# Kernel optimization log

Measured on AMD Instinct MI355X. Metric: run time of the kernel, lower is better.

The kernel has to match this reference:

```python
import jax, jax.numpy as jnp
import numpy as np

B, T, D_MODEL = 2, 2048, 2048
N, H, R = 1024, 16, 512
DH = 128          # mem_head_dim (even, fully rotated: rope_dim == DH)
MLAT = 128        # mem_latent_dim
TOPK = 64
EPS = 1e-6
ROPE_BASE = 10000.0


def _rms_norm(x, w):
    var = jnp.mean(jnp.square(x), axis=-1, keepdims=True)
    return x * jax.lax.rsqrt(var + EPS) * w


def _rotate_half(x):
    x1, x2 = jnp.split(x, 2, axis=-1)
    return jnp.concatenate([-x2, x1], axis=-1)


def _apply_rope(x, positions):
    # x: [B, H, L, DH], positions: [L] -> cos/sin [1, 1, L, DH]
    inv_freq = 1.0 / (ROPE_BASE ** (jnp.arange(0, DH, 2, dtype=jnp.float32) / DH))
    freqs = positions.astype(jnp.float32)[:, None] * inv_freq  # [L, DH/2]
    emb = jnp.concatenate([freqs, freqs], axis=-1)             # [L, DH]
    cos = jnp.cos(emb)[None, None].astype(x.dtype)
    sin = jnp.sin(emb)[None, None].astype(x.dtype)
    return x * cos + _rotate_half(x) * sin


def setup_inputs() -> dict:
    key = jax.random.key(0)
    ks = jax.random.split(key, 16)
    s = 0.02
    return {
        "x": jax.random.normal(ks[0], (B, T, D_MODEL), jnp.float32),
        "snapshots": jax.random.normal(ks[1], (B, N, H, R), jnp.float32),
        "snap_positions": jnp.sort(jax.random.randint(ks[2], (N,), 0, T)),
        "token_offset": 0,
        "Wq_down": jax.random.normal(ks[3], (D_MODEL, MLAT), jnp.float32) * s,
        "Wq_up": jax.random.normal(ks[4], (MLAT, H * DH), jnp.float32) * s,
        "Wg_down": jax.random.normal(ks[5], (D_MODEL, MLAT), jnp.float32) * s,
        "Wg_up": jax.random.normal(ks[6], (MLAT, H * DH), jnp.float32) * s,
        "Wo_down": jax.random.normal(ks[7], (H * DH, MLAT), jnp.float32) * s,
        "Wo_up": jax.random.normal(ks[8], (MLAT, D_MODEL), jnp.float32) * s,
        "Wk_up": jax.random.normal(ks[9], (R, DH), jnp.float32) * s,
        "Wv_up": jax.random.normal(ks[10], (R, DH), jnp.float32) * s,
        "q_norm_w": jnp.ones((DH,), jnp.float32),
        "k_norm_w": jnp.ones((DH,), jnp.float32),
        "sink_logit": jnp.zeros((H,), jnp.float32),
    }


def reference(x, snapshots, snap_positions, token_offset,
              Wq_down, Wq_up, Wg_down, Wg_up, Wo_down, Wo_up,
              Wk_up, Wv_up, q_norm_w, k_norm_w, sink_logit):
    b, t, d = x.shape
    _, n, h, r = snapshots.shape
    dh = DH

    # Q path: down/up projection, per-head RMSNorm -> [B, H, T, DH]
    q = ((x @ Wq_down) @ Wq_up).reshape(b, t, h, dh)
    q = _rms_norm(q, q_norm_w).transpose(0, 2, 1, 3)

    # K/V from snapshot latents: [B, N, H, DH] -> [B, H, N, DH]
    k = _rms_norm(snapshots @ Wk_up, k_norm_w).transpose(0, 2, 1, 3)
    v = (snapshots @ Wv_up).transpose(0, 2, 1, 3)

    # dual RoPE: Q by absolute token position, K by snapshot end position
    t_abs = token_offset + jnp.arange(t)
    q = _apply_rope(q, t_abs)
    k = _apply_rope(k, snap_positions)

    scores = jnp.einsum('bhtd,bhnd->bhtn', q, k) / jnp.sqrt(jnp.asarray(dh, q.dtype))

    # causal mask: snapshot strictly before token
    valid = (snap_positions[None, :] < t_abs[:, None])[None, None]  # [1,1,T,N]
    neg_inf = jnp.asarray(-jnp.inf, scores.dtype)
    scores = jnp.where(valid, scores, neg_inf)

    # causal top-k: keep entries >= k-th largest per (b,h,t)
    k_sel = min(TOPK, n)
    if k_sel < n:
        top_vals, _ = jax.lax.top_k(scores, k_sel)
        kth = top_vals[..., -1:]
        scores = jnp.where(scores >= kth, scores, neg_inf)

    # attention sink: extra learned logit per head
    sink = jnp.broadcast_to(sink_logit.astype(jnp.float32)[None, :, None, None], (b, h, t, 1))
    aug = jnp.concatenate([scores.astype(jnp.float32), sink], axis=-1)
    weights = jax.nn.softmax(aug, axis=-1)[..., :n].astype(v.dtype)

    out = jnp.einsum('bhtn,bhnd->bhtd', weights, v)
    out = out.transpose(0, 2, 1, 3).reshape(b, t, h * dh)

    gate = jax.nn.sigmoid((x @ Wg_down) @ Wg_up)
    out = out * gate
    out = (out @ Wo_down) @ Wo_up
    return out
```

## Files before the change

### kernel.cpp

```cpp
#include <hip/hip_runtime.h>

typedef unsigned short u16;
typedef unsigned int u32;
typedef __attribute__((ext_vector_type(8))) short bf16x8;
typedef __attribute__((ext_vector_type(8))) _Float16 f16x8;
typedef __attribute__((ext_vector_type(4))) float f32x4;

__device__ __forceinline__ float b2f(u16 u) {
  union { u32 i; float f; } v; v.i = ((u32)u) << 16; return v.f;
}
__device__ __forceinline__ u16 f2b(float f) {
  u32 u = __builtin_bit_cast(u32, f);
  u32 r = u + 0x7FFFu + ((u >> 16) & 1u);
  return (u16)(r >> 16);
}
__device__ __forceinline__ u16 f2h(float f) {
  return __builtin_bit_cast(u16, (_Float16)f);
}
__device__ __forceinline__ float h2f(u16 u) {
  return (float)__builtin_bit_cast(_Float16, u);
}
__device__ __forceinline__ float wsum(float v) {
  #pragma unroll
  for (int o = 32; o; o >>= 1) v += __shfl_xor(v, o);
  return v;
}
__device__ __forceinline__ float wmax(float v) {
  #pragma unroll
  for (int o = 32; o; o >>= 1) v = fmaxf(v, __shfl_xor(v, o));
  return v;
}

__global__ void k_detect(const u32* x, int* flag) {
  int lane = threadIdx.x;
  u32 w = x[lane * 131 + 7];
  float v = b2f((u16)(w & 0xFFFF));
  float a = fabsf(v);
  bool sane = (a > 1e-3f) && (a < 100.0f);
  unsigned long long m = __ballot(sane);
  if (lane == 0) flag[0] = (__popcll(m) >= 32) ? 0 : 1;
}

struct WtArgs {
  const void* s[8];
  const void* vq; const void* vk; const void* vs;
};
__global__ __launch_bounds__(256)
void k_wtrans_all(WtArgs a, u16* wb, const int* flag) {
  __shared__ u16 Ts[64][66];
  int id = blockIdx.x, t = threadIdx.x, dt = flag[0];
  if (id == 416) {
    u16* dq = wb + 1703936; u16* dk = wb + 1704064; u16* ds = wb + 1704192;
    if (t < 128) dq[t] = dt ? f2b(((const float*)a.vq)[t]) : ((const u16*)a.vq)[t];
    else if (t < 256) dk[t-128] = dt ? f2b(((const float*)a.vk)[t-128]) : ((const u16*)a.vk)[t-128];
    if (t < 16) ds[t] = dt ? f2b(((const float*)a.vs)[t]) : ((const u16*)a.vs)[t];
    return;
  }
  const int cum[9] = {0,64,128,144,160,224,288,352,416};
  const int gsh[8] = {1,1,1,1,5,5,1,5};
  const int Ks[8]  = {2048,2048,512,512,128,128,2048,128};
  const int Ns[8]  = {128,128,128,128,2048,2048,128,2048};
  const unsigned dsts[8] = {0,262144,524288,589824,655360,917504,1179648,1441792};
  int seg = 0;
  #pragma unroll
  for (int i = 0; i < 7; ++i) seg += (id >= cum[i+1]);
  int rel = id - cum[seg];
  int bx = rel & ((1 << gsh[seg]) - 1), by = rel >> gsh[seg];
  int K = Ks[seg], N = Ns[seg];
  const void* src = a.s[seg];
  u16* dst = wb + dsts[seg];
  int col0 = bx * 64, k0 = by * 64;
  int lr = t >> 4, lc = (t & 15) * 4;
  if (dt) {
    #pragma unroll
    for (int p = 0; p < 4; ++p) {
      int kr = lr + p * 16;
      float4 v = *(const float4*)((const float*)src + (size_t)(k0 + kr) * N + col0 + lc);
      Ts[kr][lc+0] = f2b(v.x); Ts[kr][lc+1] = f2b(v.y);
      Ts[kr][lc+2] = f2b(v.z); Ts[kr][lc+3] = f2b(v.w);
    }
  } else {
    #pragma unroll
    for (int p = 0; p < 4; ++p) {
      int kr = lr + p * 16;
      uint2 v = *(const uint2*)((const u16*)src + (size_t)(k0 + kr) * N + col0 + lc);
      *(uint2*)&Ts[kr][lc] = v;
    }
  }
  __syncthreads();
  int col = t >> 2, ks = (t & 3) * 16;
  u16 tmp[16];
  #pragma unroll
  for (int i = 0; i < 16; ++i) tmp[i] = Ts[ks + i][col];
  u16* dp = dst + (size_t)(col0 + col) * K + k0 + ks;
  *(uint4*)dp = *(uint4*)&tmp[0];
  *(uint4*)(dp + 8) = *(uint4*)&tmp[8];
}

template<int JW>
__device__ __forceinline__ void skinny_body(const void* A, const u16* BT, u16* C0, u16* C1,
    int K, bool a32, int m0, int tid, u16 (*As)[40]) {
  int wave = tid >> 6, lane = tid & 63, quad = lane >> 4, l16 = lane & 15;
  f32x4 acc[JW];
  #pragma unroll
  for (int j = 0; j < JW; ++j) acc[j] = (f32x4){0.f,0.f,0.f,0.f};
  int row32 = tid >> 4, kp32 = (tid & 15) * 2;
  int row16 = tid >> 2, kp16 = (tid & 3) * 8;
  float2 pf32 = {};
  uint4 pf16 = {};
  if (a32) pf32 = *(const float2*)((const float*)A + (size_t)(m0+row32)*K + kp32);
  else if (tid < 64) pf16 = *(const uint4*)((const u16*)A + (size_t)(m0+row16)*K + kp16);
  uint4 bf[JW];
  #pragma unroll
  for (int j = 0; j < JW; ++j) {
    int col = wave*(JW*16) + j*16 + l16;
    bf[j] = *(const uint4*)(BT + (size_t)col*K + quad*8);
  }
  for (int k0 = 0; k0 < K; k0 += 32) {
    if (a32) { As[row32][kp32] = f2b(pf32.x); As[row32][kp32+1] = f2b(pf32.y); }
    else if (tid < 64) *(uint4*)&As[row16][kp16] = pf16;
    __syncthreads();
    int k1 = k0 + 32;
    uint4 bn[JW];
    if (k1 < K) {
      if (a32) pf32 = *(const float2*)((const float*)A + (size_t)(m0+row32)*K + k1 + kp32);
      else if (tid < 64) pf16 = *(const uint4*)((const u16*)A + (size_t)(m0+row16)*K + k1 + kp16);
      #pragma unroll
      for (int j = 0; j < JW; ++j) {
        int col = wave*(JW*16) + j*16 + l16;
        bn[j] = *(const uint4*)(BT + (size_t)col*K + k1 + quad*8);
      }
    }
    bf16x8 af = *(const bf16x8*)&As[l16][quad*8];
    #pragma unroll
    for (int j = 0; j < JW; ++j)
      acc[j] = __builtin_amdgcn_mfma_f32_16x16x32_bf16(af, __builtin_bit_cast(bf16x8, bf[j]), acc[j], 0, 0, 0);
    __syncthreads();
    #pragma unroll
    for (int j = 0; j < JW; ++j) bf[j] = bn[j];
  }
  #pragma unroll
  for (int j = 0; j < JW; ++j) {
    int col = wave*(JW*16) + j*16 + l16;
    u16* Cp = (col < 128) ? C0 : C1;
    int cc = col & 127;
    #pragma unroll
    for (int r = 0; r < 4; ++r)
      Cp[(size_t)(m0 + quad*4 + r)*128 + cc] = f2b(acc[j][r]);
  }
}

__device__ __forceinline__ void gemm_up_body(const u16* A, const u16* BT, void* C, int ldc,
    bool o32, int m0, int n0, int tid, u16 (*As)[40]) {
  int wave = tid >> 6, lane = tid & 63, quad = lane >> 4, l16 = lane & 15;
  f32x4 acc[4] = {};
  int row = tid >> 2, kp = (tid & 3) * 8;
  uint4 pa = *(const uint4*)(A + (size_t)(m0+row)*128 + kp);
  uint4 bf[4];
  #pragma unroll
  for (int j = 0; j < 4; ++j)
    bf[j] = *(const uint4*)(BT + (size_t)(n0 + j*16 + l16)*128 + quad*8);
  #pragma unroll
  for (int k0 = 0; k0 < 128; k0 += 32) {
    *(uint4*)&As[row][kp] = pa;
    __syncthreads();
    uint4 bn[4];
    if (k0 < 96) {
      pa = *(const uint4*)(A + (size_t)(m0+row)*128 + k0 + 32 + kp);
      #pragma unroll
      for (int j = 0; j < 4; ++j)
        bn[j] = *(const uint4*)(BT + (size_t)(n0 + j*16 + l16)*128 + k0 + 32 + quad*8);
    }
    bf16x8 af = *(const bf16x8*)&As[wave*16 + l16][quad*8];
    #pragma unroll
    for (int j = 0; j < 4; ++j)
      acc[j] = __builtin_amdgcn_mfma_f32_16x16x32_bf16(af, __builtin_bit_cast(bf16x8, bf[j]), acc[j], 0, 0, 0);
    __syncthreads();
    #pragma unroll
    for (int j = 0; j < 4; ++j) bf[j] = bn[j];
  }
  #pragma unroll
  for (int j = 0; j < 4; ++j) {
    #pragma unroll
    for (int r = 0; r < 4; ++r) {
      size_t ci = (size_t)(m0 + wave*16 + quad*4 + r)*ldc + n0 + j*16 + l16;
      float v = acc[j][r];
      if (o32) ((float*)C)[ci] = v; else ((u16*)C)[ci] = f2b(v);
    }
  }
}

__device__ __forceinline__ void kpost_body(const u16* kraw, u16* kT, const u16* kw,
                                           const int* spos, int rel, int tid) {
  int wave = tid >> 6, lane = tid & 63;
  int rr = rel * 4 + wave;
  int n = (rr >> 4) & 1023, b = rr >> 14, h = rr & 15;
  size_t base = (size_t)rr * 128;
  float x0 = b2f(kraw[base + lane]);
  float x1 = b2f(kraw[base + lane + 64]);
  float ss = wsum(x0*x0 + x1*x1);
  float inv = rsqrtf(ss * (1.0f/128.0f) + 1e-6f);
  float y0 = x0 * inv * b2f(kw[lane]);
  float y1 = x1 * inv * b2f(kw[lane + 64]);
  float pos = (float)spos[n];
  float invf = __expf(-(float)lane * (9.210340371976184f / 64.0f));
  float sn, cs; sincosf(pos * invf, &sn, &cs);
  size_t ob = ((size_t)(b*16 + h) * 1024 + n) * 128;
  kT[ob + lane]      = f2b(y0*cs - y1*sn);
  kT[ob + lane + 64] = f2b(y1*cs + y0*sn);
}

__device__ __forceinline__ void vtrans_body(const u16* vraw, u16* vtt, int bid, int t,
                                            u16 (*Vs)[136]) {
  int ng = bid & 15, bh = bid >> 4;
  int b = bh >> 4, h = bh & 15;
  int n0 = ng * 64;
  int li = t >> 4, seg = (t & 15) * 8;
  #pragma unroll
  for (int p = 0; p < 4; ++p) {
    int i = li + p * 16;
    size_t row = (size_t)(b*1024 + n0 + i) * 16 + h;
    *(uint4*)&Vs[i][seg] = *(const uint4*)(vraw + row*128 + seg);
  }
  __syncthreads();
  int dh = t >> 1, nh = (t & 1) * 32;
  u16 outv[32];
  #pragma unroll
  for (int i = 0; i < 32; ++i) outv[i] = f2h(b2f(Vs[nh + i][dh]));
  u16* dst = vtt + ((size_t)bh * 128 + dh) * 1024 + n0 + nh;
  *(uint4*)(dst)      = *(uint4*)&outv[0];
  *(uint4*)(dst + 8)  = *(uint4*)&outv[8];
  *(uint4*)(dst + 16) = *(uint4*)&outv[16];
  *(uint4*)(dst + 24) = *(uint4*)&outv[24];
}

__global__ __launch_bounds__(256)
void k_down_all(const void* x, const void* snap, const u16* BdT, const u16* BkvT,
                u16* qlat, u16* glat, u16* kraw, u16* vraw, const int* flag) {
  __shared__ u16 As[16][40];
  int id = blockIdx.x;
  bool a32 = flag[0] != 0;
  if (id < 256) skinny_body<4>(x, BdT, qlat, glat, 2048, a32, id*16, threadIdx.x, As);
  else          skinny_body<4>(snap, BkvT, kraw, vraw, 512, a32, (id-256)*16, threadIdx.x, As);
}

__global__ __launch_bounds__(256)
void k_mid_all(const u16* qlat, const u16* glat, const u16* WquT, const u16* WguT,
               u16* qraw, u16* graw, const u16* kraw, u16* kT, const u16* vraw, u16* vtt,
               const u16* ckw, const int* spos, const int* flag) {
  __shared__ u16 smem[64*136];
  int id = blockIdx.x, tid = threadIdx.x;
  if (id < 4096) {
    u16 (*As)[40] = (u16 (*)[40])smem;
    int rel = id & 2047;
    const u16* A  = (id < 2048) ? qlat : glat;
    const u16* BT = (id < 2048) ? WquT : WguT;
    u16* C        = (id < 2048) ? qraw : graw;
    gemm_up_body(A, BT, C, 2048, false, (rel >> 5) * 64, (rel & 31) * 64, tid, As);
  } else if (id < 12288) {
    kpost_body(kraw, kT, ckw, spos, id - 4096, tid);
  } else {
    vtrans_body(vraw, vtt, id - 12288, tid, (u16 (*)[136])smem);
  }
}

__global__ __launch_bounds__(256)
void k_olat(const u16* Ao, const u16* WodT, u16* olat, const int* flag) {
  __shared__ u16 As[16][40];
  skinny_body<2>(Ao, WodT, olat, olat, 2048, false, blockIdx.x*16, threadIdx.x, As);
}

__global__ __launch_bounds__(256)
void k_gemm_up(const u16* A, const u16* BT, void* C, int ldc, const int* flag, int out_dyn) {
  __shared__ u16 As[64][40];
  gemm_up_body(A, BT, C, ldc, out_dyn && flag[0], blockIdx.y*64, blockIdx.x*64, threadIdx.x, As);
}

__global__ __launch_bounds__(256, 4)
void k_attn(const u16* qraw, const u16* kT, const u16* vtt, const u16* graw,
            const int* spos, const int* tok, const u16* sink, const u16* qw, u16* o) {
  __shared__ u16 sc[16][1032];
  __shared__ int pos_s[1024];
  __shared__ float rz_s[16];
  u16 (*Qs)[136] = (u16 (*)[136])&sc[0][0];

  int tid = threadIdx.x;
  int wave = tid >> 6, lane = tid & 63, quad = lane >> 4, l16 = lane & 15;
  int bid = blockIdx.x;
  int tile = bid & 127, bh = bid >> 7;
  int h = bh & 15, b = bh >> 4;
  int t0 = tile * 16;
  int tok0 = tok[0];

  ((int4*)pos_s)[tid] = ((const int4*)spos)[tid];

  {
    float qw0 = b2f(qw[lane]), qw1 = b2f(qw[lane + 64]);
    float invf = __expf(-(float)lane * (9.210340371976184f / 64.0f));
    #pragma unroll 1
    for (int s = 0; s < 4; ++s) {
      int i = wave*4 + s;
      size_t base = ((size_t)(b*2048 + t0 + i))*2048 + h*128;
      float x0 = b2f(qraw[base + lane]);
      float x1 = b2f(qraw[base + lane + 64]);
      float ss = wsum(x0*x0 + x1*x1);
      float inv = rsqrtf(ss * (1.0f/128.0f) + 1e-6f);
      float y0 = x0 * inv * qw0;
      float y1 = x1 * inv * qw1;
      float pos = (float)(tok0 + t0 + i);
      float sn, cs; sincosf(pos * invf, &sn, &cs);
      Qs[i][lane]      = f2b(y0*cs - y1*sn);
      Qs[i][lane + 64] = f2b(y1*cs + y0*sn);
    }
  }
  __syncthreads();

  int nmax;
  {
    int lim = tok0 + t0 + 15;
    int lo = 0, hi = 1024;
    #pragma unroll 1
    while (lo < hi) { int mid = (lo + hi) >> 1; if (pos_s[mid] < lim) lo = mid + 1; else hi = mid; }
    nmax = lo;
  }
  int pmax = (nmax + 63) >> 6;
  int kkmax = (nmax + 31) >> 5;

  bf16x8 af[4];
  #pragma unroll
  for (int ks = 0; ks < 4; ++ks) af[ks] = *(const bf16x8*)&Qs[l16][ks*32 + quad*8];
  __syncthreads();

  const u16* kTb = kT + (size_t)bh * 131072;
  int nrow = wave*16 + l16;
  uint4 kf[4];
  if (pmax > 0) {
    const u16* kr = kTb + (size_t)nrow * 128 + quad*8;
    #pragma unroll
    for (int ks = 0; ks < 4; ++ks) kf[ks] = *(const uint4*)(kr + ks*32);
  }
  #pragma unroll 1
  for (int p = 0; p < pmax; ++p) {
    uint4 kn[4];
    if (p + 1 < pmax) {
      const u16* kr = kTb + (size_t)((p+1)*64 + nrow) * 128 + quad*8;
      #pragma unroll
      for (int ks = 0; ks < 4; ++ks) kn[ks] = *(const uint4*)(kr + ks*32);
    }
    f32x4 c = {};
    #pragma unroll
    for (int ks = 0; ks < 4; ++ks)
      c = __builtin_amdgcn_mfma_f32_16x16x32_bf16(af[ks], __builtin_bit_cast(bf16x8, kf[ks]), c, 0, 0, 0);
    int n = p*64 + nrow;
    int pn = pos_s[n];
    #pragma unroll
    for (int r = 0; r < 4; ++r) {
      int t = quad*4 + r;
      float s = c[r] * 0.08838834764831845f;
      if (pn >= tok0 + t0 + t) s = -INFINITY;
      sc[t][n] = f2h(s);
    }
    #pragma unroll
    for (int ks = 0; ks < 4; ++ks) kf[ks] = kn[ks];
  }
  #pragma unroll 1
  for (int p = pmax; p < 16; ++p) {
    int n = p*64 + nrow;
    #pragma unroll
    for (int r = 0; r < 4; ++r) sc[quad*4 + r][n] = 0xFC00u;
  }
  __syncthreads();

  float sinkv = b2f(sink[h]);

  #pragma unroll 1
  for (int s5 = 0; s5 < 4; ++s5) {
    int tl = wave*4 + s5;
    uint4 r0 = *(const uint4*)&sc[tl][lane*16];
    uint4 r1 = *(const uint4*)&sc[tl][lane*16 + 8];
    float sv[16]; int key[16];
    float mx = -INFINITY;
    #pragma unroll
    for (int j = 0; j < 16; ++j) {
      u16 hb = (j < 8) ? ((const u16*)&r0)[j] : ((const u16*)&r1)[j-8];
      float f = h2f(hb);
      sv[j] = f; mx = fmaxf(mx, f);
      float fs = fminf(fmaxf(f * 256.0f + 2048.0f, 0.0f), 4095.0f);
      key[j] = (int)fs;
    }
    mx = wmax(mx);
    int lo = 0, hi = 4096;
    #pragma unroll 1
    for (int it = 0; it < 12; ++it) {
      int mid = (lo + hi) >> 1;
      int c = 0;
      #pragma unroll
      for (int j = 0; j < 16; ++j) c += (int)__popcll(__ballot(key[j] >= mid));
      if (c >= 64) lo = mid; else hi = mid;
    }
    float m = fmaxf(mx, sinkv);
    float zp = 0.f;
    u16 wq[16];
    #pragma unroll
    for (int j = 0; j < 16; ++j) {
      float e = (key[j] >= lo && sv[j] > -1e37f) ? __expf(sv[j] - m) : 0.f;
      zp += e;
      wq[j] = f2h(e);
    }
    float Z = wsum(zp) + __expf(sinkv - m);
    if (lane == 0) rz_s[tl] = 1.0f / Z;
    *(uint4*)&sc[tl][lane*16]     = *(uint4*)&wq[0];
    *(uint4*)&sc[tl][lane*16 + 8] = *(uint4*)&wq[8];
  }
  __syncthreads();

  const u16* vbase = vtt + (size_t)bh * 131072;
  int dh0 = wave * 32;
  const u16* vr0 = vbase + (size_t)(dh0 + l16)*1024 + quad*8;
  const u16* vr1 = vbase + (size_t)(dh0 + 16 + l16)*1024 + quad*8;
  f32x4 acc0 = {}, acc1 = {};
  uint4 vf0 = *(const uint4*)vr0;
  uint4 vf1 = *(const uint4*)vr1;
  #pragma unroll 1
  for (int kk = 0; kk < kkmax; ++kk) {
    uint4 vn0, vn1;
    if (kk + 1 < kkmax) {
      vn0 = *(const uint4*)(vr0 + (kk+1)*32);
      vn1 = *(const uint4*)(vr1 + (kk+1)*32);
    }
    f16x8 a = *(const f16x8*)&sc[l16][kk*32 + quad*8];
    acc0 = __builtin_amdgcn_mfma_f32_16x16x32_f16(a, __builtin_bit_cast(f16x8, vf0), acc0, 0, 0, 0);
    acc1 = __builtin_amdgcn_mfma_f32_16x16x32_f16(a, __builtin_bit_cast(f16x8, vf1), acc1, 0, 0, 0);
    vf0 = vn0; vf1 = vn1;
  }

  #pragma unroll
  for (int r = 0; r < 4; ++r) {
    int t = quad*4 + r;
    float rz = rz_s[t];
    size_t oi = ((size_t)(b*2048 + t0 + t))*2048 + h*128 + dh0 + l16;
    float g0 = 1.0f / (1.0f + __expf(-b2f(graw[oi])));
    float g1 = 1.0f / (1.0f + __expf(-b2f(graw[oi + 16])));
    o[oi] = f2b(acc0[r] * rz * g0);
    o[oi + 16] = f2b(acc1[r] * rz * g1);
  }
}

extern "C" void kernel_launch(void* const* d_in, const int* in_sizes, int n_in,
                              void* d_out, int out_size, void* d_ws, size_t ws_size,
                              hipStream_t stream) {
  char* ws = (char*)d_ws;
  int* flag = (int*)(ws + 0);
  u16* wb = (u16*)(ws + 4096);

  u16* BdT  = wb + 0;
  u16* BkvT = wb + 524288;
  u16* WquT = wb + 655360;
  u16* WguT = wb + 917504;
  u16* WodT = wb + 1179648;
  u16* WouT = wb + 1441792;
  u16* cqw  = wb + 1703936;
  u16* ckw  = wb + 1704064;
  u16* csink= wb + 1704192;

  const size_t O_QLAT = 4198400;
  const size_t O_GLAT = 5246976;
  const size_t O_QRAW = 6295552;
  const size_t O_GRAW = 23072768;
  const size_t O_KRAW = 39849984;
  const size_t O_VRAW = 48238592;
  const size_t O_KT   = 56627200;
  const size_t O_VTT  = 65015808;

  const int* spos = (const int*)d_in[2];
  const int* tok  = (const int*)d_in[3];

  k_detect<<<1, 64, 0, stream>>>((const u32*)d_in[0], flag);

  WtArgs wa;
  wa.s[0] = d_in[4];  wa.s[1] = d_in[6];  wa.s[2] = d_in[10]; wa.s[3] = d_in[11];
  wa.s[4] = d_in[5];  wa.s[5] = d_in[7];  wa.s[6] = d_in[8];  wa.s[7] = d_in[9];
  wa.vq = d_in[12]; wa.vk = d_in[13]; wa.vs = d_in[14];
  k_wtrans_all<<<417, 256, 0, stream>>>(wa, wb, flag);

  k_down_all<<<2304, 256, 0, stream>>>(d_in[0], d_in[1], BdT, BkvT,
      (u16*)(ws + O_QLAT), (u16*)(ws + O_GLAT), (u16*)(ws + O_KRAW), (u16*)(ws + O_VRAW), flag);

  k_mid_all<<<12800, 256, 0, stream>>>((const u16*)(ws + O_QLAT), (const u16*)(ws + O_GLAT),
      WquT, WguT, (u16*)(ws + O_QRAW), (u16*)(ws + O_GRAW),
      (const u16*)(ws + O_KRAW), (u16*)(ws + O_KT), (const u16*)(ws + O_VRAW), (u16*)(ws + O_VTT),
      ckw, spos, flag);

  k_attn<<<4096, 256, 0, stream>>>((const u16*)(ws + O_QRAW), (const u16*)(ws + O_KT),
      (const u16*)(ws + O_VTT), (const u16*)(ws + O_GRAW), spos, tok, csink, cqw,
      (u16*)(ws + O_GRAW));

  k_olat<<<256, 256, 0, stream>>>((const u16*)(ws + O_GRAW), WodT, (u16*)(ws + O_QLAT), flag);
  k_gemm_up<<<dim3(32,64), 256, 0, stream>>>((const u16*)(ws + O_QLAT), WouT, d_out, 2048, flag, 1);
}
```

Measured before the change: 533.1 us.

## Swizzle attention score LDS layout, interleave topk rows, remap blocks, set MFMA priority

Replaces the padded score buffer in shared memory with an unpadded XOR-swizzled layout to avoid bank conflicts while keeping the footprint small. The explicit fill of masked tail columns is replaced by predicating columns beyond nmax to -inf when rows are loaded. The top-k binary search now processes two rows per wave together, interleaving their ballots and reductions for more instruction-level parallelism. Block indices are remapped so neighbouring blocks spread across batch/head, and MFMA sections are wrapped in s_setprio. These add index arithmetic and register pressure, which could affect occupancy.

```diff
diff --git a/kernel.cpp b/kernel.cpp
--- a/kernel.cpp
+++ b/kernel.cpp
@@ -279,14 +279,16 @@
 __global__ __launch_bounds__(256, 4)
 void k_attn(const u16* qraw, const u16* kT, const u16* vtt, const u16* graw,
             const int* spos, const int* tok, const u16* sink, const u16* qw, u16* o) {
-  __shared__ u16 sc[16][1032];
+  __shared__ u16 sc[16*1024];
   __shared__ int pos_s[1024];
   __shared__ float rz_s[16];
-  u16 (*Qs)[136] = (u16 (*)[136])&sc[0][0];
+  char* scB = (char*)sc;
+  u16 (*Qs)[136] = (u16 (*)[136])sc;
 
   int tid = threadIdx.x;
   int wave = tid >> 6, lane = tid & 63, quad = lane >> 4, l16 = lane & 15;
-  int bid = blockIdx.x;
+  int bid0 = blockIdx.x;
+  int bid = (bid0 & 7) * 512 + (bid0 >> 3);
   int tile = bid & 127, bh = bid >> 7;
   int h = bh & 15, b = bh >> 4;
   int t0 = tile * 16;
@@ -339,6 +341,7 @@
     #pragma unroll
     for (int ks = 0; ks < 4; ++ks) kf[ks] = *(const uint4*)(kr + ks*32);
   }
+  int lim0 = tok0 + t0;
   #pragma unroll 1
   for (int p = 0; p < pmax; ++p) {
     uint4 kn[4];
@@ -348,69 +351,104 @@
       for (int ks = 0; ks < 4; ++ks) kn[ks] = *(const uint4*)(kr + ks*32);
     }
     f32x4 c = {};
+    __builtin_amdgcn_s_setprio(1);
     #pragma unroll
     for (int ks = 0; ks < 4; ++ks)
       c = __builtin_amdgcn_mfma_f32_16x16x32_bf16(af[ks], __builtin_bit_cast(bf16x8, kf[ks]), c, 0, 0, 0);
+    __builtin_amdgcn_s_setprio(0);
     int n = p*64 + nrow;
     int pn = pos_s[n];
     #pragma unroll
     for (int r = 0; r < 4; ++r) {
       int t = quad*4 + r;
       float s = c[r] * 0.08838834764831845f;
-      if (pn >= tok0 + t0 + t) s = -INFINITY;
-      sc[t][n] = f2h(s);
+      if (pn >= lim0 + t) s = -INFINITY;
+      *(u16*)(scB + ((t*2048 + n*2) ^ ((t&7)<<4))) = f2h(s);
     }
     #pragma unroll
     for (int ks = 0; ks < 4; ++ks) kf[ks] = kn[ks];
   }
+  __syncthreads();
+
+  float sinkv = b2f(sink[h]);
+
+  int tl0 = wave*4;
+  int c0 = lane*8;
   #pragma unroll 1
-  for (int p = pmax; p < 16; ++p) {
-    int n = p*64 + nrow;
-    #pragma unroll
-    for (int r = 0; r < 4; ++r) sc[quad*4 + r][n] = 0xFC00u;
-  }
-  __syncthreads();
-
-  float sinkv = b2f(sink[h]);
-
-  #pragma unroll 1
-  for (int s5 = 0; s5 < 4; ++s5) {
-    int tl = wave*4 + s5;
-    uint4 r0 = *(const uint4*)&sc[tl][lane*16];
-    uint4 r1 = *(const uint4*)&sc[tl][lane*16 + 8];
-    float sv[16]; int key[16];
-    float mx = -INFINITY;
-    #pragma unroll
-    for (int j = 0; j < 16; ++j) {
-      u16 hb = (j < 8) ? ((const u16*)&r0)[j] : ((const u16*)&r1)[j-8];
-      float f = h2f(hb);
-      sv[j] = f; mx = fmaxf(mx, f);
-      float fs = fminf(fmaxf(f * 256.0f + 2048.0f, 0.0f), 4095.0f);
-      key[j] = (int)fs;
-    }
-    mx = wmax(mx);
-    int lo = 0, hi = 4096;
+  for (int half = 0; half < 2; ++half) {
+    float sv[2][16]; int key[2][16];
+    #pragma unroll
+    for (int s2 = 0; s2 < 2; ++s2) {
+      int tl = tl0 + half*2 + s2;
+      int sxor = (tl&7) << 4;
+      const char* rowp = scB + tl*2048;
+      uint4 r0 = *(const uint4*)(rowp + ((lane*16) ^ sxor));
+      uint4 r1 = *(const uint4*)(rowp + (1024 + ((lane*16) ^ sxor)));
+      #pragma unroll
+      for (int j = 0; j < 8; ++j) {
+        sv[s2][j]   = (c0 + j       < nmax) ? h2f(((const u16*)&r0)[j]) : -INFINITY;
+        sv[s2][j+8] = (c0 + j + 512 < nmax) ? h2f(((const u16*)&r1)[j]) : -INFINITY;
+      }
+    }
+    float mx[2];
+    #pragma unroll
+    for (int s2 = 0; s2 < 2; ++s2) {
+      float m = -INFINITY;
+      #pragma unroll
+      for (int j = 0; j < 16; ++j) {
+        float f = sv[s2][j];
+        m = fmaxf(m, f);
+        float fs = fminf(fmaxf(f * 256.0f + 2048.0f, 0.0f), 4095.0f);
+        key[s2][j] = (int)fs;
+      }
+      mx[s2] = m;
+    }
+    #pragma unroll
+    for (int os = 32; os; os >>= 1) {
+      #pragma unroll
+      for (int s2 = 0; s2 < 2; ++s2) mx[s2] = fmaxf(mx[s2], __shfl_xor(mx[s2], os));
+    }
+    int lo2[2] = {0, 0}, hi2[2] = {4096, 4096};
     #pragma unroll 1
     for (int it = 0; it < 12; ++it) {
-      int mid = (lo + hi) >> 1;
-      int c = 0;
-      #pragma unroll
-      for (int j = 0; j < 16; ++j) c += (int)__popcll(__ballot(key[j] >= mid));
-      if (c >= 64) lo = mid; else hi = mid;
-    }
-    float m = fmaxf(mx, sinkv);
-    float zp = 0.f;
-    u16 wq[16];
-    #pragma unroll
-    for (int j = 0; j < 16; ++j) {
-      float e = (key[j] >= lo && sv[j] > -1e37f) ? __expf(sv[j] - m) : 0.f;
-      zp += e;
-      wq[j] = f2h(e);
-    }
-    float Z = wsum(zp) + __expf(sinkv - m);
-    if (lane == 0) rz_s[tl] = 1.0f / Z;
-    *(uint4*)&sc[tl][lane*16]     = *(uint4*)&wq[0];
-    *(uint4*)&sc[tl][lane*16 + 8] = *(uint4*)&wq[8];
+      #pragma unroll
+      for (int s2 = 0; s2 < 2; ++s2) {
+        int mid = (lo2[s2] + hi2[s2]) >> 1;
+        int c = 0;
+        #pragma unroll
+        for (int j = 0; j < 16; ++j) c += (int)__popcll(__ballot(key[s2][j] >= mid));
+        if (c >= 64) lo2[s2] = mid; else hi2[s2] = mid;
+      }
+    }
+    float m2[2], zp[2];
+    u16 wq[2][16];
+    #pragma unroll
+    for (int s2 = 0; s2 < 2; ++s2) {
+      m2[s2] = fmaxf(mx[s2], sinkv);
+      float z = 0.f;
+      #pragma unroll
+      for (int j = 0; j < 16; ++j) {
+        float e = (key[s2][j] >= lo2[s2] && sv[s2][j] > -1e37f) ? __expf(sv[s2][j] - m2[s2]) : 0.f;
+        z += e;
+        wq[s2][j] = f2h(e);
+      }
+      zp[s2] = z;
+    }
+    #pragma unroll
+    for (int os = 32; os; os >>= 1) {
+      #pragma unroll
+      for (int s2 = 0; s2 < 2; ++s2) zp[s2] += __shfl_xor(zp[s2], os);
+    }
+    #pragma unroll
+    for (int s2 = 0; s2 < 2; ++s2) {
+      int tl = tl0 + half*2 + s2;
+      float Z = zp[s2] + __expf(sinkv - m2[s2]);
+      if (lane == 0) rz_s[tl] = 1.0f / Z;
+      int sxor = (tl&7) << 4;
+      char* rowp = scB + tl*2048;
+      *(uint4*)(rowp + ((lane*16) ^ sxor))        = *(uint4*)&wq[s2][0];
+      *(uint4*)(rowp + (1024 + ((lane*16) ^ sxor))) = *(uint4*)&wq[s2][8];
+    }
   }
   __syncthreads();
 
@@ -421,6 +459,8 @@
   f32x4 acc0 = {}, acc1 = {};
   uint4 vf0 = *(const uint4*)vr0;
   uint4 vf1 = *(const uint4*)vr1;
+  int axor = (l16&7) << 4;
+  const char* arow = scB + l16*2048;
   #pragma unroll 1
   for (int kk = 0; kk < kkmax; ++kk) {
     uint4 vn0, vn1;
@@ -428,9 +468,11 @@
       vn0 = *(const uint4*)(vr0 + (kk+1)*32);
       vn1 = *(const uint4*)(vr1 + (kk+1)*32);
     }
-    f16x8 a = *(const f16x8*)&sc[l16][kk*32 + quad*8];
+    f16x8 a = *(const f16x8*)(arow + ((kk*64 + quad*16) ^ axor));
+    __builtin_amdgcn_s_setprio(1);
     acc0 = __builtin_amdgcn_mfma_f32_16x16x32_f16(a, __builtin_bit_cast(f16x8, vf0), acc0, 0, 0, 0);
     acc1 = __builtin_amdgcn_mfma_f32_16x16x32_f16(a, __builtin_bit_cast(f16x8, vf1), acc1, 0, 0, 0);
+    __builtin_amdgcn_s_setprio(0);
     vf0 = vn0; vf1 = vn1;
   }
 
```

Result: faster. 521.9 us (-2.1%).
